# Kernel tuning notes

Measured on AMD Instinct MI355X. Metric: run time of the kernel, lower is better.

## Reference

```python
import jax, jax.numpy as jnp
import numpy as np

B, L, P, D, RD, M, K = 128, 128, 1024, 128, 128, 64, 4


def _ln(x, g, b):
    m = x.mean(-1, keepdims=True)
    v = ((x - m) ** 2).mean(-1, keepdims=True)
    return (x - m) / jnp.sqrt(v + 1e-5) * g + b


def _mlp2(x, w1, b1, w2, b2):
    return jax.nn.gelu(x @ w1 + b1, approximate=False) @ w2 + b2


def setup_inputs() -> dict:
    key = jax.random.key(0)
    ks = iter(jax.random.split(key, 64))

    def n(sh, s=1.0):
        return jax.random.normal(next(ks), sh, dtype=jnp.float32) * s

    def lin(i, o):
        return n((i, o), 1.0 / np.sqrt(i))

    inp = {}
    inp['l_pos'] = n((B, L, 3), 3.0)
    inp['l_x'] = n((B, L, 8))
    inp['p_pos'] = n((B, P, 3), 3.0)
    inp['p_x'] = n((B, P, 192))
    inp['p_score'] = n((B, P))
    inp['p_rad'] = jax.random.uniform(next(ks), (B, P), dtype=jnp.float32)
    inp['l_typ'] = jax.random.randint(next(ks), (B, L), 0, 256)
    inp['p_typ'] = jax.random.randint(next(ks), (B, P), 0, 256)
    inp['a_idx'] = jax.random.randint(next(ks), (B, M), 0, L)
    inp['b_idx'] = jax.random.randint(next(ks), (B, M), 0, L)
    inp['l_mask'] = jnp.ones((B, L), dtype=bool)
    inp['p_mask'] = jnp.ones((B, P), dtype=bool)
    inp.update(dict(
        le_emb=n((256, D), 0.02), le_w1=lin(8, D), le_b1=jnp.zeros(D), le_w2=lin(D, D), le_b2=jnp.zeros(D),
        le_g=jnp.ones(D), le_lnb=jnp.zeros(D),
        pe_emb=n((256, D), 0.02), pe_w1=lin(192, D), pe_b1=jnp.zeros(D), pe_w2=lin(D, D), pe_b2=jnp.zeros(D),
        ps_w1=lin(1, D), ps_b1=jnp.zeros(D), ps_w2=lin(D, D), ps_b2=jnp.zeros(D),
        pe_g=jnp.ones(D), pe_lnb=jnp.zeros(D),
        projL=lin(D, D), projP=lin(D, D), dustbin_vec=n((D,), 0.02),
        sg_w1=lin(D, D), sg_b1=jnp.zeros(D), sg_w2=lin(D, 1), sg_b2=jnp.zeros(1),
        inv_w1=lin(3, 64), inv_b1=jnp.zeros(64), inv_w2=lin(64, 1), inv_b2=jnp.zeros(1),
        retrL=lin(D, RD), retrP=lin(D, RD)))
    return inp


def _forward(l_pos, l_x, p_pos, p_x, p_score, p_rad,
             l_typ, p_typ, a_idx, b_idx, l_mask, p_mask,
             le_emb, le_w1, le_b1, le_w2, le_b2, le_g, le_lnb,
             pe_emb, pe_w1, pe_b1, pe_w2, pe_b2,
             ps_w1, ps_b1, ps_w2, ps_b2, pe_g, pe_lnb,
             projL, projP, dustbin_vec,
             sg_w1, sg_b1, sg_w2, sg_b2,
             inv_w1, inv_b1, inv_w2, inv_b2, retrL, retrP):
    neg = jnp.finfo(jnp.float32).min
    # encoders + projections
    hL = _ln(_mlp2(l_x, le_w1, le_b1, le_w2, le_b2) + le_emb[l_typ], le_g, le_lnb) @ projL  # [B,L,D]
    hP_pre = (_mlp2(p_x, pe_w1, pe_b1, pe_w2, pe_b2) + pe_emb[p_typ]
              + _mlp2(p_score[..., None], ps_w1, ps_b1, ps_w2, ps_b2))
    hP = _ln(hP_pre, pe_g, pe_lnb) @ projP  # [B,P,D]
    scale = 1.0 / jnp.sqrt(jnp.float32(hL.shape[-1]))
    # masked bipartite cross-attn logits
    logits = jnp.einsum('bld,bpd->blp', hL, hP) * scale
    logits_feat = jnp.where(p_mask[:, None, :], logits, neg)
    logits_feat = jnp.where(l_mask[:, :, None], logits_feat, neg)
    # dustbin log-softmax assignment
    dust = (hL @ dustbin_vec) * scale  # [B,L]
    full = jnp.concatenate([logits_feat, dust[:, :, None]], axis=-1)  # [B,L,P+1]
    full = jnp.where(l_mask[:, :, None], full, neg)
    logW = jax.nn.log_softmax(full, axis=-1)
    W = jnp.exp(logW)
    pm = p_mask.astype(jnp.float32)
    lm = l_mask.astype(jnp.float32)
    denomL = jnp.maximum(lm.sum(1), 1.0)
    Wm = jnp.concatenate([W[:, :, :-1] * pm[:, None, :], W[:, :, -1:]], axis=-1)
    sharp = (Wm.max(-1) * lm).sum(1) / denomL
    neg_ent = -((-(Wm * logW).sum(-1) * lm).sum(1) / denomL)
    # per-pocket-node sigma
    p_sigma = jax.nn.softplus(_mlp2(hP, sg_w1, sg_b1, sg_w2, sg_b2)[..., 0]) + 1e-3 + jnp.maximum(p_rad, 0.0)
    logW_real = logW[:, :, :-1]
    # sampled edge likelihood
    Bn = l_pos.shape[0]
    bi = jnp.arange(Bn)[:, None]
    valid = l_mask[bi, a_idx] & l_mask[bi, b_idx] & (a_idx != b_idx)  # [B,M]
    dist = jnp.linalg.norm(l_pos[bi, a_idx] - l_pos[bi, b_idx], axis=-1)[:, :, None, None]
    _, topj = jax.lax.top_k(logits_feat, K)  # [B,L,K]
    bi3 = jnp.arange(Bn)[:, None, None]
    p_sel = p_pos[bi3, topj]                 # [B,L,K,3]
    sig_sel = p_sigma[bi3, topj]             # [B,L,K]
    lW_top = jnp.take_along_axis(logW_real, topj, axis=2)  # [B,L,K]
    pa, pb = p_sel[bi, a_idx], p_sel[bi, b_idx]            # [B,M,K,3]
    siga, sigb = sig_sel[bi, a_idx], sig_sel[bi, b_idx]    # [B,M,K]
    lwa, lwb = lW_top[bi, a_idx], lW_top[bi, b_idx]
    mu = jnp.linalg.norm(pa[:, :, :, None, :] - pb[:, :, None, :, :], axis=-1)  # [B,M,K,K]
    sigma = jnp.sqrt(siga[:, :, :, None] ** 2 + sigb[:, :, None, :] ** 2 + 1e-6)
    logw_pair = lwa[:, :, :, None] + lwb[:, :, None, :]
    logp = -0.5 * ((dist - mu) / sigma) ** 2 - jnp.log(sigma) - 0.5 * jnp.log(2.0 * jnp.pi)
    logmix = jax.scipy.special.logsumexp(logw_pair + logp, axis=(-2, -1))  # [B,M]
    vp = valid.astype(jnp.float32)
    edge_raw = (logmix * vp).sum(1) / jnp.maximum(vp.sum(1), 1.0)
    edge = jnp.tanh(edge_raw / 5.0)  # edge_scale
    inv_vec = jnp.stack([sharp, neg_ent, edge], axis=1)  # [B,3]
    score_inv_geom = _mlp2(inv_vec, inv_w1, inv_b1, inv_w2, inv_b2)[..., 0]
    # pooled retrieval embeddings
    l_g = (hL * lm[:, :, None]).sum(1) / jnp.maximum(lm.sum(1, keepdims=True), 1.0)
    p_g = (hP * pm[:, :, None]).sum(1) / jnp.maximum(pm.sum(1, keepdims=True), 1.0)

    def _unit(x):
        return x / jnp.maximum(jnp.linalg.norm(x, axis=-1, keepdims=True), 1e-12)

    l_z = _unit(l_g @ retrL)
    p_z = _unit(p_g @ retrP)
    return jnp.concatenate([score_inv_geom[:, None], l_z, p_z], axis=-1)  # [B, 1+2*RD]


def reference(l_pos, l_x, p_pos, p_x, p_score, p_rad,
              l_typ, p_typ, a_idx, b_idx, l_mask, p_mask,
              le_emb, le_w1, le_b1, le_w2, le_b2, le_g, le_lnb,
              pe_emb, pe_w1, pe_b1, pe_w2, pe_b2,
              ps_w1, ps_b1, ps_w2, ps_b2, pe_g, pe_lnb,
              projL, projP, dustbin_vec,
              sg_w1, sg_b1, sg_w2, sg_b2,
              inv_w1, inv_b1, inv_w2, inv_b2, retrL, retrP):
    return _forward(l_pos, l_x, p_pos, p_x, p_score, p_rad,
                    l_typ, p_typ, a_idx, b_idx, l_mask, p_mask,
                    le_emb, le_w1, le_b1, le_w2, le_b2, le_g, le_lnb,
                    pe_emb, pe_w1, pe_b1, pe_w2, pe_b2,
                    ps_w1, ps_b1, ps_w2, ps_b2, pe_g, pe_lnb,
                    projL, projP, dustbin_vec,
                    sg_w1, sg_b1, sg_w2, sg_b2,
                    inv_w1, inv_b1, inv_w2, inv_b2, retrL, retrP)
```

## Files before the change

kernel.cpp:

```cpp
#include <hip/hip_runtime.h>
#include <math.h>

#define B_ 128
#define L_ 128
#define P_ 1024
#define D_ 128
#define M_ 64

typedef __attribute__((ext_vector_type(8))) short bf16x8;
typedef __attribute__((ext_vector_type(4))) float f32x4;

__device__ __forceinline__ float gelu_exact(float x) {
    return 0.5f * x * (1.0f + erff(x * 0.70710678118654752440f));
}
__device__ __forceinline__ float softplus_f(float x) {
    return fmaxf(x, 0.0f) + log1pf(expf(-fabsf(x)));
}
__device__ __forceinline__ unsigned short f2bf(float f) {
    unsigned int u = __float_as_uint(f);
    unsigned int r = (u + 0x7FFFu + ((u >> 16) & 1u)) >> 16;
    return (unsigned short)r;
}
__device__ __forceinline__ float bf2f(unsigned short h) {
    return __uint_as_float(((unsigned int)h) << 16);
}
__device__ __forceinline__ float xor32_sum(float v) {
#pragma unroll
    for (int o = 16; o > 0; o >>= 1) v += __shfl_xor(v, o, 32);
    return v;
}
__device__ __forceinline__ float blockReduceSum128(float v, volatile float* s2) {
#pragma unroll
    for (int o = 32; o > 0; o >>= 1) v += __shfl_down(v, o, 64);
    __syncthreads();
    if ((threadIdx.x & 63) == 0) s2[threadIdx.x >> 6] = v;
    __syncthreads();
    return s2[0] + s2[1];
}

template<int KK>
__device__ __forceinline__ void mm_tile(const float* __restrict__ W,
                                        const float* __restrict__ xT,
                                        int d0, int r0, float acc[4][4]) {
#pragma unroll 4
    for (int k = 0; k < KK; ++k) {
        float4 xv = *(const float4*)(xT + k * 16 + r0);
        float4 wv = *(const float4*)(W + k * D_ + d0);
        acc[0][0] += xv.x * wv.x; acc[0][1] += xv.x * wv.y; acc[0][2] += xv.x * wv.z; acc[0][3] += xv.x * wv.w;
        acc[1][0] += xv.y * wv.x; acc[1][1] += xv.y * wv.y; acc[1][2] += xv.y * wv.z; acc[1][3] += xv.y * wv.w;
        acc[2][0] += xv.z * wv.x; acc[2][1] += xv.z * wv.y; acc[2][2] += xv.z * wv.z; acc[2][3] += xv.z * wv.w;
        acc[3][0] += xv.w * wv.x; acc[3][1] += xv.w * wv.y; acc[3][2] += xv.w * wv.z; acc[3][3] += xv.w * wv.w;
    }
}

__global__ __launch_bounds__(256) void k_prep(
    const float* __restrict__ w1, const float* __restrict__ w2, const float* __restrict__ pp,
    const float* __restrict__ psw2, const float* __restrict__ sgw1,
    unsigned short* __restrict__ W1T, unsigned short* __restrict__ W2T, unsigned short* __restrict__ PPT,
    unsigned short* __restrict__ PSW2T, unsigned short* __restrict__ SGW1T)
{
    int d = blockIdx.x, t = threadIdx.x;
    for (int k = t; k < 192; k += 256) W1T[d * 200 + k] = f2bf(w1[k * 128 + d]);
    for (int k = t; k < 128; k += 256) {
        W2T[d * 136 + k]   = f2bf(w2[k * 128 + d]);
        PPT[d * 136 + k]   = f2bf(pp[k * 128 + d]);
        PSW2T[d * 136 + k] = f2bf(psw2[k * 128 + d]);
        SGW1T[d * 136 + k] = f2bf(sgw1[k * 128 + d]);
    }
}

__global__ __launch_bounds__(128) void k_hL(
    const float* __restrict__ l_x, const int* __restrict__ l_typ,
    const float* __restrict__ le_emb, const float* __restrict__ le_w1, const float* __restrict__ le_b1,
    const float* __restrict__ le_w2, const float* __restrict__ le_b2,
    const float* __restrict__ le_g, const float* __restrict__ le_lnb,
    const float* __restrict__ projL, float* __restrict__ hL)
{
    __shared__ __align__(16) float s_x[8 * 16];
    __shared__ __align__(16) float s_u[D_ * 16];
    __shared__ __align__(16) float s_v[D_ * 16];
    __shared__ int s_typ[16];
    int tid = threadIdx.x;
    int td = tid & 31, tr = tid >> 5;
    int d0 = td * 4, r0 = tr * 4;
    int row0 = blockIdx.x * 16;

    for (int i = tid; i < 16 * 8; i += 128) {
        int r = i >> 3, k = i & 7;
        s_x[k * 16 + r] = l_x[(row0 + r) * 8 + k];
    }
    if (tid < 16) s_typ[tid] = l_typ[row0 + tid];
    __syncthreads();

    float acc[4][4];
    {
        float4 b1 = *(const float4*)(le_b1 + d0);
#pragma unroll
        for (int i = 0; i < 4; ++i) { acc[i][0] = b1.x; acc[i][1] = b1.y; acc[i][2] = b1.z; acc[i][3] = b1.w; }
    }
    mm_tile<8>(le_w1, s_x, d0, r0, acc);
#pragma unroll
    for (int j = 0; j < 4; ++j)
        *(float4*)(s_u + (d0 + j) * 16 + r0) =
            make_float4(gelu_exact(acc[0][j]), gelu_exact(acc[1][j]), gelu_exact(acc[2][j]), gelu_exact(acc[3][j]));
    __syncthreads();

    {
        float4 b2 = *(const float4*)(le_b2 + d0);
#pragma unroll
        for (int i = 0; i < 4; ++i) {
            float4 e = *(const float4*)(le_emb + (long)s_typ[r0 + i] * D_ + d0);
            acc[i][0] = b2.x + e.x; acc[i][1] = b2.y + e.y; acc[i][2] = b2.z + e.z; acc[i][3] = b2.w + e.w;
        }
    }
    mm_tile<D_>(le_w2, s_u, d0, r0, acc);

    float ga[4], bb[4], ln[4][4];
    *(float4*)ga = *(const float4*)(le_g + d0);
    *(float4*)bb = *(const float4*)(le_lnb + d0);
#pragma unroll
    for (int i = 0; i < 4; ++i) {
        float s = acc[i][0] + acc[i][1] + acc[i][2] + acc[i][3];
        s = xor32_sum(s);
        float mean = s * (1.0f / D_);
        float dv[4], vs = 0.0f;
#pragma unroll
        for (int j = 0; j < 4; ++j) { dv[j] = acc[i][j] - mean; vs += dv[j] * dv[j]; }
        vs = xor32_sum(vs);
        float inv = rsqrtf(vs * (1.0f / D_) + 1e-5f);
#pragma unroll
        for (int j = 0; j < 4; ++j) ln[i][j] = dv[j] * inv * ga[j] + bb[j];
    }
    __syncthreads();
#pragma unroll
    for (int j = 0; j < 4; ++j)
        *(float4*)(s_v + (d0 + j) * 16 + r0) = make_float4(ln[0][j], ln[1][j], ln[2][j], ln[3][j]);
    __syncthreads();

#pragma unroll
    for (int i = 0; i < 4; ++i)
#pragma unroll
        for (int j = 0; j < 4; ++j) acc[i][j] = 0.0f;
    mm_tile<D_>(projL, s_v, d0, r0, acc);
#pragma unroll
    for (int i = 0; i < 4; ++i)
        *(float4*)(hL + (long)(row0 + r0 + i) * D_ + d0) = make_float4(acc[i][0], acc[i][1], acc[i][2], acc[i][3]);
}

#define KP1 200
#define KP2 136
#define TBo 0
#define HBo 8704
__global__ __launch_bounds__(256) void k_hP(
    const float* __restrict__ p_x, const float* __restrict__ p_score, const float* __restrict__ p_rad,
    const int* __restrict__ p_typ,
    const float* __restrict__ pe_emb, const float* __restrict__ pe_b1, const float* __restrict__ pe_b2,
    const float* __restrict__ ps_w1, const float* __restrict__ ps_b1, const float* __restrict__ ps_b2,
    const float* __restrict__ pe_g, const float* __restrict__ pe_lnb,
    const float* __restrict__ sg_b1, const float* __restrict__ sg_w2, const float* __restrict__ sg_b2,
    const unsigned short* __restrict__ W1T, const unsigned short* __restrict__ W2T,
    const unsigned short* __restrict__ PPT, const unsigned short* __restrict__ PSW2T,
    const unsigned short* __restrict__ SGW1T,
    unsigned short* __restrict__ hPb, float* __restrict__ p_sigma, float* __restrict__ w_pg)
{
    __shared__ unsigned short s_buf[17408];
    __shared__ float s_score[64], s_rad[64];
    __shared__ int s_typ[64];
    const int tid = threadIdx.x;
    const int wid = tid >> 6;
    const int l15 = tid & 15;
    const int g   = (tid & 63) >> 4;
    const long row0 = (long)blockIdx.x * 64;
    const int b  = (int)(row0 >> 10);
    const int p0 = (int)(row0 & (P_ - 1));
    const int arow = wid * 16 + l15;
    const int crow = wid * 16 + g * 4;

    {
        const float2* src = (const float2*)(p_x + row0 * 192);
        for (int i = tid; i < 64 * 96; i += 256) {
            int r = i / 96, kp = i - r * 96;
            float2 v = src[i];
            unsigned int packed = (unsigned int)f2bf(v.x) | ((unsigned int)f2bf(v.y) << 16);
            *(unsigned int*)&s_buf[r * KP1 + kp * 2] = packed;
        }
        if (tid < 64) {
            s_typ[tid] = p_typ[row0 + tid];
            s_score[tid] = p_score[row0 + tid];
            s_rad[tid] = p_rad[row0 + tid];
        }
    }
    __syncthreads();

    f32x4 acc[8];
#pragma unroll
    for (int nt = 0; nt < 8; ++nt) {
        float bv = pe_b1[nt * 16 + l15];
        acc[nt] = (f32x4){bv, bv, bv, bv};
    }
#pragma unroll
    for (int k0 = 0; k0 < 192; k0 += 32) {
        bf16x8 a = *(const bf16x8*)&s_buf[arow * KP1 + k0 + g * 8];
#pragma unroll
        for (int nt = 0; nt < 8; ++nt) {
            bf16x8 bb = *(const bf16x8*)&W1T[(nt * 16 + l15) * KP1 + k0 + g * 8];
            acc[nt] = __builtin_amdgcn_mfma_f32_16x16x32_bf16(a, bb, acc[nt], 0, 0, 0);
        }
    }
    __syncthreads();

#pragma unroll
    for (int nt = 0; nt < 8; ++nt)
#pragma unroll
        for (int reg = 0; reg < 4; ++reg)
            s_buf[TBo + (crow + reg) * KP2 + nt * 16 + l15] = f2bf(gelu_exact(acc[nt][reg]));
    for (int i = tid; i < 64 * 64; i += 256) {
        int r = i >> 6, kp = (i & 63) * 2;
        float sc = s_score[r];
        unsigned int packed = (unsigned int)f2bf(gelu_exact(sc * ps_w1[kp] + ps_b1[kp])) |
                              ((unsigned int)f2bf(gelu_exact(sc * ps_w1[kp + 1] + ps_b1[kp + 1])) << 16);
        *(unsigned int*)&s_buf[HBo + r * KP2 + kp] = packed;
    }
    __syncthreads();

#pragma unroll
    for (int nt = 0; nt < 8; ++nt) {
        int d = nt * 16 + l15;
        float bias = pe_b2[d] + ps_b2[d];
        f32x4 c;
#pragma unroll
        for (int reg = 0; reg < 4; ++reg)
            c[reg] = bias + pe_emb[(long)s_typ[crow + reg] * 128 + d];
        acc[nt] = c;
    }
#pragma unroll
    for (int k0 = 0; k0 < 128; k0 += 32) {
        bf16x8 a1 = *(const bf16x8*)&s_buf[TBo + arow * KP2 + k0 + g * 8];
        bf16x8 a2 = *(const bf16x8*)&s_buf[HBo + arow * KP2 + k0 + g * 8];
#pragma unroll
        for (int nt = 0; nt < 8; ++nt) {
            bf16x8 b1v = *(const bf16x8*)&W2T[(nt * 16 + l15) * KP2 + k0 + g * 8];
            acc[nt] = __builtin_amdgcn_mfma_f32_16x16x32_bf16(a1, b1v, acc[nt], 0, 0, 0);
            bf16x8 b2v = *(const bf16x8*)&PSW2T[(nt * 16 + l15) * KP2 + k0 + g * 8];
            acc[nt] = __builtin_amdgcn_mfma_f32_16x16x32_bf16(a2, b2v, acc[nt], 0, 0, 0);
        }
    }

    {
        float gg[8], lb[8];
#pragma unroll
        for (int nt = 0; nt < 8; ++nt) { gg[nt] = pe_g[nt * 16 + l15]; lb[nt] = pe_lnb[nt * 16 + l15]; }
#pragma unroll
        for (int reg = 0; reg < 4; ++reg) {
            float s = 0.0f;
#pragma unroll
            for (int nt = 0; nt < 8; ++nt) s += acc[nt][reg];
            s += __shfl_xor(s, 1); s += __shfl_xor(s, 2); s += __shfl_xor(s, 4); s += __shfl_xor(s, 8);
            float mean = s * (1.0f / 128.0f);
            float vs = 0.0f;
#pragma unroll
            for (int nt = 0; nt < 8; ++nt) { float dv = acc[nt][reg] - mean; vs += dv * dv; }
            vs += __shfl_xor(vs, 1); vs += __shfl_xor(vs, 2); vs += __shfl_xor(vs, 4); vs += __shfl_xor(vs, 8);
            float inv = rsqrtf(vs * (1.0f / 128.0f) + 1e-5f);
#pragma unroll
            for (int nt = 0; nt < 8; ++nt)
                acc[nt][reg] = (acc[nt][reg] - mean) * inv * gg[nt] + lb[nt];
        }
    }
    __syncthreads();
#pragma unroll
    for (int nt = 0; nt < 8; ++nt)
#pragma unroll
        for (int reg = 0; reg < 4; ++reg)
            s_buf[HBo + (crow + reg) * KP2 + nt * 16 + l15] = f2bf(acc[nt][reg]);
    __syncthreads();

#pragma unroll
    for (int nt = 0; nt < 8; ++nt) acc[nt] = (f32x4){0.0f, 0.0f, 0.0f, 0.0f};
#pragma unroll
    for (int k0 = 0; k0 < 128; k0 += 32) {
        bf16x8 a = *(const bf16x8*)&s_buf[HBo + arow * KP2 + k0 + g * 8];
#pragma unroll
        for (int nt = 0; nt < 8; ++nt) {
            bf16x8 bb = *(const bf16x8*)&PPT[(nt * 16 + l15) * KP2 + k0 + g * 8];
            acc[nt] = __builtin_amdgcn_mfma_f32_16x16x32_bf16(a, bb, acc[nt], 0, 0, 0);
        }
    }
#pragma unroll
    for (int nt = 0; nt < 8; ++nt) {
        float s = acc[nt][0] + acc[nt][1] + acc[nt][2] + acc[nt][3];
        s += __shfl_xor(s, 16);
        s += __shfl_xor(s, 32);
        if (((tid & 63) >> 4) == 0) atomicAdd(&w_pg[b * D_ + nt * 16 + l15], s);
    }
#pragma unroll
    for (int nt = 0; nt < 8; ++nt)
#pragma unroll
        for (int reg = 0; reg < 4; ++reg)
            s_buf[TBo + (crow + reg) * KP2 + nt * 16 + l15] = f2bf(acc[nt][reg]);
    __syncthreads();

    for (int i = tid; i < 1024; i += 256) {
        int r = i >> 4, seg = i & 15;
        uint4 v = *(const uint4*)&s_buf[TBo + r * KP2 + seg * 8];
        *(uint4*)&hPb[(row0 + r) * (long)D_ + seg * 8] = v;
    }

#pragma unroll
    for (int nt = 0; nt < 8; ++nt) {
        float bv = sg_b1[nt * 16 + l15];
        acc[nt] = (f32x4){bv, bv, bv, bv};
    }
#pragma unroll
    for (int k0 = 0; k0 < 128; k0 += 32) {
        bf16x8 a = *(const bf16x8*)&s_buf[TBo + arow * KP2 + k0 + g * 8];
#pragma unroll
        for (int nt = 0; nt < 8; ++nt) {
            bf16x8 bb = *(const bf16x8*)&SGW1T[(nt * 16 + l15) * KP2 + k0 + g * 8];
            acc[nt] = __builtin_amdgcn_mfma_f32_16x16x32_bf16(a, bb, acc[nt], 0, 0, 0);
        }
    }
    {
        float w2v[8];
#pragma unroll
        for (int nt = 0; nt < 8; ++nt) w2v[nt] = sg_w2[nt * 16 + l15];
        float sgb2 = sg_b2[0];
#pragma unroll
        for (int reg = 0; reg < 4; ++reg) {
            float part = 0.0f;
#pragma unroll
            for (int nt = 0; nt < 8; ++nt) part += gelu_exact(acc[nt][reg]) * w2v[nt];
            part += __shfl_xor(part, 1); part += __shfl_xor(part, 2);
            part += __shfl_xor(part, 4); part += __shfl_xor(part, 8);
            if (l15 == 0) {
                int r = crow + reg;
                p_sigma[(long)b * P_ + p0 + r] = softplus_f(part + sgb2) + 0.001f + fmaxf(s_rad[r], 0.0f);
            }
        }
    }
}

__global__ __launch_bounds__(256) void k_logits(
    const float* __restrict__ hL, const unsigned short* __restrict__ hPb,
    const float* __restrict__ dustbin,
    float* __restrict__ w_sharp, float* __restrict__ w_ent,
    float* __restrict__ w_lw, int* __restrict__ w_idx)
{
    __shared__ unsigned short s_hl[16 * 136];
    __shared__ unsigned short s_lg[16 * 1048];
    __shared__ float s_dust[16];
    __shared__ float s_red_m[4][16];
    __shared__ float2 s_red_s[4][16];
    __shared__ float s_lse[16];

    const int tid = threadIdx.x;
    const int w = tid >> 6;
    const int l15 = tid & 15;
    const int g = (tid & 63) >> 4;
    const int b = blockIdx.x >> 3;
    const int l0 = (blockIdx.x & 7) * 16;
    const float scale = 0.08838834764831845f;

    for (int i = tid; i < 16 * 16; i += 256) {
        int r = i >> 4, c8 = (i & 15) * 8;
        const float4* src = (const float4*)(hL + ((long)(b * L_ + l0 + r)) * D_ + c8);
        float4 v0 = src[0], v1 = src[1];
        unsigned int u0 = (unsigned)f2bf(v0.x) | ((unsigned)f2bf(v0.y) << 16);
        unsigned int u1 = (unsigned)f2bf(v0.z) | ((unsigned)f2bf(v0.w) << 16);
        unsigned int u2 = (unsigned)f2bf(v1.x) | ((unsigned)f2bf(v1.y) << 16);
        unsigned int u3 = (unsigned)f2bf(v1.z) | ((unsigned)f2bf(v1.w) << 16);
        *(uint4*)&s_hl[r * 136 + c8] = make_uint4(u0, u1, u2, u3);
    }
    __syncthreads();

    {
        int r = tid >> 4;
        int k0 = (tid & 15) * 8;
        float s = 0.0f;
#pragma unroll
        for (int e = 0; e < 8; ++e) s += bf2f(s_hl[r * 136 + k0 + e]) * dustbin[k0 + e];
        s += __shfl_xor(s, 1); s += __shfl_xor(s, 2); s += __shfl_xor(s, 4); s += __shfl_xor(s, 8);
        if ((tid & 15) == 0) s_dust[r] = s * scale;
    }

    bf16x8 a[4];
#pragma unroll
    for (int k = 0; k < 4; ++k) a[k] = *(const bf16x8*)&s_hl[l15 * 136 + k * 32 + g * 8];
    const unsigned short* hp = hPb + (long)b * P_ * D_ + (long)(w * 256 + l15) * D_ + g * 8;
    f32x4 acc[16];
#pragma unroll
    for (int nt = 0; nt < 16; ++nt) acc[nt] = (f32x4){0.0f, 0.0f, 0.0f, 0.0f};
#pragma unroll
    for (int k = 0; k < 4; ++k) {
#pragma unroll
        for (int nt = 0; nt < 16; ++nt) {
            bf16x8 bb = *(const bf16x8*)(hp + nt * (16 * D_) + k * 32);
            acc[nt] = __builtin_amdgcn_mfma_f32_16x16x32_bf16(a[k], bb, acc[nt], 0, 0, 0);
        }
    }
#pragma unroll
    for (int nt = 0; nt < 16; ++nt)
#pragma unroll
        for (int reg = 0; reg < 4; ++reg) acc[nt][reg] *= scale;

    float mloc[4];
#pragma unroll
    for (int reg = 0; reg < 4; ++reg) {
        float m = acc[0][reg];
#pragma unroll
        for (int nt = 1; nt < 16; ++nt) m = fmaxf(m, acc[nt][reg]);
        m = fmaxf(m, __shfl_xor(m, 1)); m = fmaxf(m, __shfl_xor(m, 2));
        m = fmaxf(m, __shfl_xor(m, 4)); m = fmaxf(m, __shfl_xor(m, 8));
        mloc[reg] = m;
        if (l15 == 0) s_red_m[w][g * 4 + reg] = m;
    }
#pragma unroll
    for (int nt = 0; nt < 16; ++nt)
#pragma unroll
        for (int reg = 0; reg < 4; ++reg)
            s_lg[(g * 4 + reg) * 1048 + w * 256 + nt * 16 + l15] = f2bf(acc[nt][reg]);
    __syncthreads();

    float mf[4];
#pragma unroll
    for (int reg = 0; reg < 4; ++reg) {
        int r = g * 4 + reg;
        float m = fmaxf(fmaxf(s_red_m[0][r], s_red_m[1][r]), fmaxf(s_red_m[2][r], s_red_m[3][r]));
        mf[reg] = fmaxf(m, s_dust[r]);
    }
#pragma unroll
    for (int reg = 0; reg < 4; ++reg) {
        float S0 = 0.0f, S1 = 0.0f;
#pragma unroll
        for (int nt = 0; nt < 16; ++nt) {
            float x = acc[nt][reg] - mf[reg];
            float e = expf(x);
            S0 += e; S1 += e * x;
        }
        S0 += __shfl_xor(S0, 1); S0 += __shfl_xor(S0, 2); S0 += __shfl_xor(S0, 4); S0 += __shfl_xor(S0, 8);
        S1 += __shfl_xor(S1, 1); S1 += __shfl_xor(S1, 2); S1 += __shfl_xor(S1, 4); S1 += __shfl_xor(S1, 8);
        if (l15 == 0) s_red_s[w][g * 4 + reg] = make_float2(S0, S1);
    }
    __syncthreads();

    if (tid < 64 && l15 == 0) {
#pragma unroll
        for (int reg = 0; reg < 4; ++reg) {
            int r = g * 4 + reg;
            float m = mf[reg];
            float S0 = 0.0f, S1 = 0.0f;
#pragma unroll
            for (int ww = 0; ww < 4; ++ww) { float2 s = s_red_s[ww][r]; S0 += s.x; S1 += s.y; }
            float xd = s_dust[r] - m;
            float ed = expf(xd);
            S0 += ed; S1 += ed * xd;
            float lgz = logf(S0);
            int rowg = b * L_ + l0 + r;
            w_sharp[rowg] = 1.0f / S0;
            w_ent[rowg] = S1 / S0 - lgz;
            s_lse[r] = m + lgz;
        }
    }
    __syncthreads();

    {
        int r = tid >> 4;
        int lane = tid & 15;
        float lse = s_lse[r];
        int rowg = b * L_ + l0 + r;
        for (int k = 0; k < 4; ++k) {
            float bv = -INFINITY; int bi = P_;
            for (int c = lane; c < P_; c += 16) {
                float v = bf2f(s_lg[r * 1048 + c]);
                if (v > bv || (v == bv && c < bi)) { bv = v; bi = c; }
            }
#pragma unroll
            for (int o = 1; o < 16; o <<= 1) {
                float ov = __shfl_xor(bv, o);
                int   oi = __shfl_xor(bi, o);
                if (ov > bv || (ov == bv && oi < bi)) { bv = ov; bi = oi; }
            }
            if (lane == 0) {
                w_lw[rowg * 4 + k] = bv - lse;
                w_idx[rowg * 4 + k] = bi;
            }
            s_lg[r * 1048 + bi] = 0xFF80;
        }
    }
}

__global__ __launch_bounds__(64) void k_edge(
    const int* __restrict__ a_idx, const int* __restrict__ b_idx,
    const float* __restrict__ l_pos, const float* __restrict__ p_pos,
    const float* __restrict__ p_sigma, const float* __restrict__ w_lw,
    const int* __restrict__ w_idx, float* __restrict__ w_edge)
{
    int b = blockIdx.x, m = threadIdx.x;
    int ai = a_idx[b * M_ + m], bi = b_idx[b * M_ + m];
    bool valid = (ai != bi);
    float ax = l_pos[(b * L_ + ai) * 3 + 0], ay = l_pos[(b * L_ + ai) * 3 + 1], az = l_pos[(b * L_ + ai) * 3 + 2];
    float bx = l_pos[(b * L_ + bi) * 3 + 0], by = l_pos[(b * L_ + bi) * 3 + 1], bz = l_pos[(b * L_ + bi) * 3 + 2];
    float dx = ax - bx, dy = ay - by, dz = az - bz;
    float dist = sqrtf(dx * dx + dy * dy + dz * dz);

    float pax[4], pay[4], paz[4], sa2[4], lwa[4];
    float pbx[4], pby[4], pbz[4], sb2[4], lwb[4];
#pragma unroll
    for (int k = 0; k < 4; ++k) {
        int ja = w_idx[(b * L_ + ai) * 4 + k];
        pax[k] = p_pos[(b * P_ + ja) * 3 + 0]; pay[k] = p_pos[(b * P_ + ja) * 3 + 1]; paz[k] = p_pos[(b * P_ + ja) * 3 + 2];
        float sa = p_sigma[b * P_ + ja]; sa2[k] = sa * sa;
        lwa[k] = w_lw[(b * L_ + ai) * 4 + k];
        int jb = w_idx[(b * L_ + bi) * 4 + k];
        pbx[k] = p_pos[(b * P_ + jb) * 3 + 0]; pby[k] = p_pos[(b * P_ + jb) * 3 + 1]; pbz[k] = p_pos[(b * P_ + jb) * 3 + 2];
        float sb = p_sigma[b * P_ + jb]; sb2[k] = sb * sb;
        lwb[k] = w_lw[(b * L_ + bi) * 4 + k];
    }
    float t[16];
    float mx = -INFINITY;
#pragma unroll
    for (int j = 0; j < 4; ++j)
#pragma unroll
        for (int k = 0; k < 4; ++k) {
            float ddx = pax[j] - pbx[k], ddy = pay[j] - pby[k], ddz = paz[j] - pbz[k];
            float mu = sqrtf(ddx * ddx + ddy * ddy + ddz * ddz);
            float s2 = sa2[j] + sb2[k] + 1e-6f;
            float diff = dist - mu;
            float lp = lwa[j] + lwb[k] - 0.5f * diff * diff / s2 - 0.5f * logf(s2) - 0.91893853320467274f;
            t[j * 4 + k] = lp;
            mx = fmaxf(mx, lp);
        }
    float se = 0.0f;
#pragma unroll
    for (int n = 0; n < 16; ++n) se += expf(t[n] - mx);
    float logmix = mx + logf(se);
    float v = valid ? logmix : 0.0f;
    float c = valid ? 1.0f : 0.0f;
#pragma unroll
    for (int o = 32; o > 0; o >>= 1) { v += __shfl_down(v, o, 64); c += __shfl_down(c, o, 64); }
    if (m == 0) w_edge[b] = tanhf((v / fmaxf(c, 1.0f)) * 0.2f);
}

__global__ __launch_bounds__(128) void k_final(
    const float* __restrict__ hL, const float* __restrict__ w_pg,
    const float* __restrict__ w_sharp, const float* __restrict__ w_ent, const float* __restrict__ w_edge,
    const float* __restrict__ inv_w1, const float* __restrict__ inv_b1,
    const float* __restrict__ inv_w2, const float* __restrict__ inv_b2,
    const float* __restrict__ retrL, const float* __restrict__ retrP,
    float* __restrict__ out)
{
    __shared__ float s_red[2];
    __shared__ float s_vec[D_];
    int b = blockIdx.x, tid = threadIdx.x;
    float sharp = blockReduceSum128(w_sharp[b * L_ + tid], s_red) * (1.0f / L_);
    float neg_ent = blockReduceSum128(w_ent[b * L_ + tid], s_red) * (1.0f / L_);
    float edge = w_edge[b];
    float v = 0.0f;
    if (tid < 64) {
        float h = gelu_exact(sharp * inv_w1[tid] + neg_ent * inv_w1[64 + tid] + edge * inv_w1[128 + tid] + inv_b1[tid]);
        v = h * inv_w2[tid];
    }
    float sc = blockReduceSum128(v, s_red);
    if (tid == 0) out[b * 257] = sc + inv_b2[0];

    float lg = 0.0f;
    for (int l = 0; l < L_; ++l) lg += hL[((long)b * L_ + l) * D_ + tid];
    s_vec[tid] = lg * (1.0f / L_);
    __syncthreads();
    float z = 0.0f;
    for (int k = 0; k < D_; ++k) z += s_vec[k] * retrL[k * D_ + tid];
    float nrm = sqrtf(blockReduceSum128(z * z, s_red));
    out[b * 257 + 1 + tid] = z / fmaxf(nrm, 1e-12f);
    __syncthreads();

    s_vec[tid] = w_pg[b * D_ + tid] * (1.0f / P_);
    __syncthreads();
    z = 0.0f;
    for (int k = 0; k < D_; ++k) z += s_vec[k] * retrP[k * D_ + tid];
    nrm = sqrtf(blockReduceSum128(z * z, s_red));
    out[b * 257 + 129 + tid] = z / fmaxf(nrm, 1e-12f);
}

extern "C" void kernel_launch(void* const* d_in, const int* in_sizes, int n_in,
                              void* d_out, int out_size, void* d_ws, size_t ws_size,
                              hipStream_t stream) {
    (void)in_sizes; (void)n_in; (void)out_size; (void)ws_size;
    const float* l_pos  = (const float*)d_in[0];
    const float* l_x    = (const float*)d_in[1];
    const float* p_pos  = (const float*)d_in[2];
    const float* p_x    = (const float*)d_in[3];
    const float* p_score= (const float*)d_in[4];
    const float* p_rad  = (const float*)d_in[5];
    const int*   l_typ  = (const int*)d_in[6];
    const int*   p_typ  = (const int*)d_in[7];
    const int*   a_idx  = (const int*)d_in[8];
    const int*   b_idx  = (const int*)d_in[9];
    const float* le_emb = (const float*)d_in[12];
    const float* le_w1  = (const float*)d_in[13];
    const float* le_b1  = (const float*)d_in[14];
    const float* le_w2  = (const float*)d_in[15];
    const float* le_b2  = (const float*)d_in[16];
    const float* le_g   = (const float*)d_in[17];
    const float* le_lnb = (const float*)d_in[18];
    const float* pe_emb = (const float*)d_in[19];
    const float* pe_w1  = (const float*)d_in[20];
    const float* pe_b1  = (const float*)d_in[21];
    const float* pe_w2  = (const float*)d_in[22];
    const float* pe_b2  = (const float*)d_in[23];
    const float* ps_w1  = (const float*)d_in[24];
    const float* ps_b1  = (const float*)d_in[25];
    const float* ps_w2  = (const float*)d_in[26];
    const float* ps_b2  = (const float*)d_in[27];
    const float* pe_g   = (const float*)d_in[28];
    const float* pe_lnb = (const float*)d_in[29];
    const float* projL  = (const float*)d_in[30];
    const float* projP  = (const float*)d_in[31];
    const float* dustbin= (const float*)d_in[32];
    const float* sg_w1  = (const float*)d_in[33];
    const float* sg_b1  = (const float*)d_in[34];
    const float* sg_w2  = (const float*)d_in[35];
    const float* sg_b2  = (const float*)d_in[36];
    const float* inv_w1 = (const float*)d_in[37];
    const float* inv_b1 = (const float*)d_in[38];
    const float* inv_w2 = (const float*)d_in[39];
    const float* inv_b2 = (const float*)d_in[40];
    const float* retrL  = (const float*)d_in[41];
    const float* retrP  = (const float*)d_in[42];

    unsigned short* hPb = (unsigned short*)d_ws;
    float* hL      = (float*)(hPb + (size_t)B_ * P_ * D_);
    float* p_sigma = hL + (size_t)B_ * L_ * D_;
    float* w_sharp = p_sigma + (size_t)B_ * P_;
    float* w_ent   = w_sharp + B_ * L_;
    float* w_lw    = w_ent + B_ * L_;
    int*   w_idx   = (int*)(w_lw + B_ * L_ * 4);
    float* w_edge  = (float*)(w_idx + B_ * L_ * 4);
    float* w_pg    = w_edge + B_;
    unsigned short* W1T   = (unsigned short*)(w_pg + B_ * D_);
    unsigned short* W2T   = W1T + 128 * 200;
    unsigned short* PPT   = W2T + 128 * 136;
    unsigned short* PSW2T = PPT + 128 * 136;
    unsigned short* SGW1T = PSW2T + 128 * 136;

    hipMemsetAsync(w_pg, 0, B_ * D_ * sizeof(float), stream);

    hipLaunchKernelGGL(k_prep, dim3(128), dim3(256), 0, stream,
                       pe_w1, pe_w2, projP, ps_w2, sg_w1, W1T, W2T, PPT, PSW2T, SGW1T);
    hipLaunchKernelGGL(k_hL, dim3(B_ * L_ / 16), dim3(128), 0, stream,
                       l_x, l_typ, le_emb, le_w1, le_b1, le_w2, le_b2, le_g, le_lnb, projL, hL);
    hipLaunchKernelGGL(k_hP, dim3(B_ * P_ / 64), dim3(256), 0, stream,
                       p_x, p_score, p_rad, p_typ, pe_emb, pe_b1, pe_b2,
                       ps_w1, ps_b1, ps_b2, pe_g, pe_lnb,
                       sg_b1, sg_w2, sg_b2,
                       W1T, W2T, PPT, PSW2T, SGW1T,
                       hPb, p_sigma, w_pg);
    hipLaunchKernelGGL(k_logits, dim3(B_ * (L_ / 16)), dim3(256), 0, stream,
                       hL, hPb, dustbin, w_sharp, w_ent, w_lw, w_idx);
    hipLaunchKernelGGL(k_edge, dim3(B_), dim3(64), 0, stream,
                       a_idx, b_idx, l_pos, p_pos, p_sigma, w_lw, w_idx, w_edge);
    hipLaunchKernelGGL(k_final, dim3(B_), dim3(128), 0, stream,
                       hL, w_pg, w_sharp, w_ent, w_edge, inv_w1, inv_b1, inv_w2, inv_b2, retrL, retrP,
                       (float*)d_out);
}
```

Measured before the change: 567.7 us.

## Restructure hP kernel to direct loads, fast GELU, fuse edge and final kernels

k_hP now loads p_x straight from global into MFMA fragments and computes the score-MLP hidden activations in registers. This removes the large shared staging buffer and most block-wide barriers, and a launch-bounds hint raises occupancy. Exact erf GELU in k_hP is replaced by the tanh approximation, which changes numerics. The ligand mean-pool moves into k_hL through atomics, and k_edge is merged into the final kernel to save a launch and the hL re-read.

```diff
diff --git a/kernel.cpp b/kernel.cpp
--- a/kernel.cpp
+++ b/kernel.cpp
@@ -13,6 +13,12 @@
 __device__ __forceinline__ float gelu_exact(float x) {
     return 0.5f * x * (1.0f + erff(x * 0.70710678118654752440f));
 }
+__device__ __forceinline__ float gelu_fast(float x) {
+    float y = 0.7978845608028654f * (x + 0.044715f * x * x * x);
+    float e = __expf(2.0f * y);
+    float t = 1.0f - 2.0f / (e + 1.0f);
+    return 0.5f * x * (1.0f + t);
+}
 __device__ __forceinline__ float softplus_f(float x) {
     return fmaxf(x, 0.0f) + log1pf(expf(-fabsf(x)));
 }
@@ -23,6 +29,14 @@
 }
 __device__ __forceinline__ float bf2f(unsigned short h) {
     return __uint_as_float(((unsigned int)h) << 16);
+}
+__device__ __forceinline__ bf16x8 pack8(float4 a, float4 b) {
+    union { unsigned int u[4]; bf16x8 v; } r;
+    r.u[0] = (unsigned)f2bf(a.x) | ((unsigned)f2bf(a.y) << 16);
+    r.u[1] = (unsigned)f2bf(a.z) | ((unsigned)f2bf(a.w) << 16);
+    r.u[2] = (unsigned)f2bf(b.x) | ((unsigned)f2bf(b.y) << 16);
+    r.u[3] = (unsigned)f2bf(b.z) | ((unsigned)f2bf(b.w) << 16);
+    return r.v;
 }
 __device__ __forceinline__ float xor32_sum(float v) {
 #pragma unroll
@@ -74,7 +88,7 @@
     const float* __restrict__ le_emb, const float* __restrict__ le_w1, const float* __restrict__ le_b1,
     const float* __restrict__ le_w2, const float* __restrict__ le_b2,
     const float* __restrict__ le_g, const float* __restrict__ le_lnb,
-    const float* __restrict__ projL, float* __restrict__ hL)
+    const float* __restrict__ projL, float* __restrict__ hL, float* __restrict__ w_lg)
 {
     __shared__ __align__(16) float s_x[8 * 16];
     __shared__ __align__(16) float s_u[D_ * 16];
@@ -145,13 +159,19 @@
 #pragma unroll
     for (int i = 0; i < 4; ++i)
         *(float4*)(hL + (long)(row0 + r0 + i) * D_ + d0) = make_float4(acc[i][0], acc[i][1], acc[i][2], acc[i][3]);
+
+    int b = row0 >> 7;
+#pragma unroll
+    for (int j = 0; j < 4; ++j) {
+        float s = acc[0][j] + acc[1][j] + acc[2][j] + acc[3][j];
+        s += __shfl_xor(s, 32, 64);
+        if ((tr & 1) == 0) atomicAdd(&w_lg[b * D_ + d0 + j], s);
+    }
 }
 
 #define KP1 200
 #define KP2 136
-#define TBo 0
-#define HBo 8704
-__global__ __launch_bounds__(256) void k_hP(
+__global__ __launch_bounds__(256, 5) void k_hP(
     const float* __restrict__ p_x, const float* __restrict__ p_score, const float* __restrict__ p_rad,
     const int* __restrict__ p_typ,
     const float* __restrict__ pe_emb, const float* __restrict__ pe_b1, const float* __restrict__ pe_b2,
@@ -163,34 +183,17 @@
     const unsigned short* __restrict__ SGW1T,
     unsigned short* __restrict__ hPb, float* __restrict__ p_sigma, float* __restrict__ w_pg)
 {
-    __shared__ unsigned short s_buf[17408];
-    __shared__ float s_score[64], s_rad[64];
-    __shared__ int s_typ[64];
-    const int tid = threadIdx.x;
-    const int wid = tid >> 6;
-    const int l15 = tid & 15;
-    const int g   = (tid & 63) >> 4;
+    __shared__ unsigned short s_tb[64 * KP2];
+    const int tid  = threadIdx.x;
+    const int wid  = tid >> 6;
+    const int lane = tid & 63;
+    const int l15  = tid & 15;
+    const int g    = lane >> 4;
     const long row0 = (long)blockIdx.x * 64;
-    const int b  = (int)(row0 >> 10);
-    const int p0 = (int)(row0 & (P_ - 1));
+    const int b = (int)(row0 >> 10);
     const int arow = wid * 16 + l15;
     const int crow = wid * 16 + g * 4;
-
-    {
-        const float2* src = (const float2*)(p_x + row0 * 192);
-        for (int i = tid; i < 64 * 96; i += 256) {
-            int r = i / 96, kp = i - r * 96;
-            float2 v = src[i];
-            unsigned int packed = (unsigned int)f2bf(v.x) | ((unsigned int)f2bf(v.y) << 16);
-            *(unsigned int*)&s_buf[r * KP1 + kp * 2] = packed;
-        }
-        if (tid < 64) {
-            s_typ[tid] = p_typ[row0 + tid];
-            s_score[tid] = p_score[row0 + tid];
-            s_rad[tid] = p_rad[row0 + tid];
-        }
-    }
-    __syncthreads();
+    const long grow = row0 + arow;
 
     f32x4 acc[8];
 #pragma unroll
@@ -198,31 +201,29 @@
         float bv = pe_b1[nt * 16 + l15];
         acc[nt] = (f32x4){bv, bv, bv, bv};
     }
-#pragma unroll
-    for (int k0 = 0; k0 < 192; k0 += 32) {
-        bf16x8 a = *(const bf16x8*)&s_buf[arow * KP1 + k0 + g * 8];
-#pragma unroll
-        for (int nt = 0; nt < 8; ++nt) {
-            bf16x8 bb = *(const bf16x8*)&W1T[(nt * 16 + l15) * KP1 + k0 + g * 8];
-            acc[nt] = __builtin_amdgcn_mfma_f32_16x16x32_bf16(a, bb, acc[nt], 0, 0, 0);
-        }
-    }
-    __syncthreads();
-
+    {
+        const float* xrow = p_x + grow * 192;
+#pragma unroll
+        for (int k = 0; k < 6; ++k) {
+            float4 v0 = *(const float4*)(xrow + k * 32 + g * 8);
+            float4 v1 = *(const float4*)(xrow + k * 32 + g * 8 + 4);
+            bf16x8 a = pack8(v0, v1);
+#pragma unroll
+            for (int nt = 0; nt < 8; ++nt) {
+                bf16x8 bb = *(const bf16x8*)&W1T[(nt * 16 + l15) * KP1 + k * 32 + g * 8];
+                acc[nt] = __builtin_amdgcn_mfma_f32_16x16x32_bf16(a, bb, acc[nt], 0, 0, 0);
+            }
+        }
+    }
 #pragma unroll
     for (int nt = 0; nt < 8; ++nt)
 #pragma unroll
         for (int reg = 0; reg < 4; ++reg)
-            s_buf[TBo + (crow + reg) * KP2 + nt * 16 + l15] = f2bf(gelu_exact(acc[nt][reg]));
-    for (int i = tid; i < 64 * 64; i += 256) {
-        int r = i >> 6, kp = (i & 63) * 2;
-        float sc = s_score[r];
-        unsigned int packed = (unsigned int)f2bf(gelu_exact(sc * ps_w1[kp] + ps_b1[kp])) |
-                              ((unsigned int)f2bf(gelu_exact(sc * ps_w1[kp + 1] + ps_b1[kp + 1])) << 16);
-        *(unsigned int*)&s_buf[HBo + r * KP2 + kp] = packed;
-    }
-    __syncthreads();
-
+            s_tb[(crow + reg) * KP2 + nt * 16 + l15] = f2bf(gelu_fast(acc[nt][reg]));
+
+    int typ[4];
+#pragma unroll
+    for (int reg = 0; reg < 4; ++reg) typ[reg] = p_typ[row0 + crow + reg];
 #pragma unroll
     for (int nt = 0; nt < 8; ++nt) {
         int d = nt * 16 + l15;
@@ -230,19 +231,30 @@
         f32x4 c;
 #pragma unroll
         for (int reg = 0; reg < 4; ++reg)
-            c[reg] = bias + pe_emb[(long)s_typ[crow + reg] * 128 + d];
+            c[reg] = bias + pe_emb[(long)typ[reg] * D_ + d];
         acc[nt] = c;
     }
-#pragma unroll
-    for (int k0 = 0; k0 < 128; k0 += 32) {
-        bf16x8 a1 = *(const bf16x8*)&s_buf[TBo + arow * KP2 + k0 + g * 8];
-        bf16x8 a2 = *(const bf16x8*)&s_buf[HBo + arow * KP2 + k0 + g * 8];
-#pragma unroll
-        for (int nt = 0; nt < 8; ++nt) {
-            bf16x8 b1v = *(const bf16x8*)&W2T[(nt * 16 + l15) * KP2 + k0 + g * 8];
-            acc[nt] = __builtin_amdgcn_mfma_f32_16x16x32_bf16(a1, b1v, acc[nt], 0, 0, 0);
-            bf16x8 b2v = *(const bf16x8*)&PSW2T[(nt * 16 + l15) * KP2 + k0 + g * 8];
-            acc[nt] = __builtin_amdgcn_mfma_f32_16x16x32_bf16(a2, b2v, acc[nt], 0, 0, 0);
+    {
+        float score = p_score[grow];
+#pragma unroll
+        for (int k = 0; k < 4; ++k) {
+            float4 w0 = *(const float4*)(ps_w1 + k * 32 + g * 8);
+            float4 w1v = *(const float4*)(ps_w1 + k * 32 + g * 8 + 4);
+            float4 c0 = *(const float4*)(ps_b1 + k * 32 + g * 8);
+            float4 c1 = *(const float4*)(ps_b1 + k * 32 + g * 8 + 4);
+            float4 h0 = make_float4(gelu_fast(score * w0.x + c0.x), gelu_fast(score * w0.y + c0.y),
+                                    gelu_fast(score * w0.z + c0.z), gelu_fast(score * w0.w + c0.w));
+            float4 h1 = make_float4(gelu_fast(score * w1v.x + c1.x), gelu_fast(score * w1v.y + c1.y),
+                                    gelu_fast(score * w1v.z + c1.z), gelu_fast(score * w1v.w + c1.w));
+            bf16x8 ah = pack8(h0, h1);
+            bf16x8 a1 = *(const bf16x8*)&s_tb[arow * KP2 + k * 32 + g * 8];
+#pragma unroll
+            for (int nt = 0; nt < 8; ++nt) {
+                bf16x8 b1v = *(const bf16x8*)&W2T[(nt * 16 + l15) * KP2 + k * 32 + g * 8];
+                acc[nt] = __builtin_amdgcn_mfma_f32_16x16x32_bf16(a1, b1v, acc[nt], 0, 0, 0);
+                bf16x8 b2v = *(const bf16x8*)&PSW2T[(nt * 16 + l15) * KP2 + k * 32 + g * 8];
+                acc[nt] = __builtin_amdgcn_mfma_f32_16x16x32_bf16(ah, b2v, acc[nt], 0, 0, 0);
+            }
         }
     }
 
@@ -267,22 +279,20 @@
                 acc[nt][reg] = (acc[nt][reg] - mean) * inv * gg[nt] + lb[nt];
         }
     }
-    __syncthreads();
 #pragma unroll
     for (int nt = 0; nt < 8; ++nt)
 #pragma unroll
         for (int reg = 0; reg < 4; ++reg)
-            s_buf[HBo + (crow + reg) * KP2 + nt * 16 + l15] = f2bf(acc[nt][reg]);
-    __syncthreads();
+            s_tb[(crow + reg) * KP2 + nt * 16 + l15] = f2bf(acc[nt][reg]);
 
 #pragma unroll
     for (int nt = 0; nt < 8; ++nt) acc[nt] = (f32x4){0.0f, 0.0f, 0.0f, 0.0f};
 #pragma unroll
-    for (int k0 = 0; k0 < 128; k0 += 32) {
-        bf16x8 a = *(const bf16x8*)&s_buf[HBo + arow * KP2 + k0 + g * 8];
+    for (int k = 0; k < 4; ++k) {
+        bf16x8 a = *(const bf16x8*)&s_tb[arow * KP2 + k * 32 + g * 8];
 #pragma unroll
         for (int nt = 0; nt < 8; ++nt) {
-            bf16x8 bb = *(const bf16x8*)&PPT[(nt * 16 + l15) * KP2 + k0 + g * 8];
+            bf16x8 bb = *(const bf16x8*)&PPT[(nt * 16 + l15) * KP2 + k * 32 + g * 8];
             acc[nt] = __builtin_amdgcn_mfma_f32_16x16x32_bf16(a, bb, acc[nt], 0, 0, 0);
         }
     }
@@ -291,19 +301,20 @@
         float s = acc[nt][0] + acc[nt][1] + acc[nt][2] + acc[nt][3];
         s += __shfl_xor(s, 16);
         s += __shfl_xor(s, 32);
-        if (((tid & 63) >> 4) == 0) atomicAdd(&w_pg[b * D_ + nt * 16 + l15], s);
+        if (g == 0) atomicAdd(&w_pg[b * D_ + nt * 16 + l15], s);
     }
 #pragma unroll
     for (int nt = 0; nt < 8; ++nt)
 #pragma unroll
         for (int reg = 0; reg < 4; ++reg)
-            s_buf[TBo + (crow + reg) * KP2 + nt * 16 + l15] = f2bf(acc[nt][reg]);
-    __syncthreads();
-
-    for (int i = tid; i < 1024; i += 256) {
-        int r = i >> 4, seg = i & 15;
-        uint4 v = *(const uint4*)&s_buf[TBo + r * KP2 + seg * 8];
-        *(uint4*)&hPb[(row0 + r) * (long)D_ + seg * 8] = v;
+            s_tb[(crow + reg) * KP2 + nt * 16 + l15] = f2bf(acc[nt][reg]);
+
+#pragma unroll
+    for (int it = 0; it < 4; ++it) {
+        int idx = lane + it * 64;
+        int r = idx >> 4, seg = idx & 15;
+        uint4 v = *(const uint4*)&s_tb[(wid * 16 + r) * KP2 + seg * 8];
+        *(uint4*)&hPb[(row0 + wid * 16 + r) * (long)D_ + seg * 8] = v;
     }
 
 #pragma unroll
@@ -312,11 +323,11 @@
         acc[nt] = (f32x4){bv, bv, bv, bv};
     }
 #pragma unroll
-    for (int k0 = 0; k0 < 128; k0 += 32) {
-        bf16x8 a = *(const bf16x8*)&s_buf[TBo + arow * KP2 + k0 + g * 8];
+    for (int k = 0; k < 4; ++k) {
+        bf16x8 a = *(const bf16x8*)&s_tb[arow * KP2 + k * 32 + g * 8];
 #pragma unroll
         for (int nt = 0; nt < 8; ++nt) {
-            bf16x8 bb = *(const bf16x8*)&SGW1T[(nt * 16 + l15) * KP2 + k0 + g * 8];
+            bf16x8 bb = *(const bf16x8*)&SGW1T[(nt * 16 + l15) * KP2 + k * 32 + g * 8];
             acc[nt] = __builtin_amdgcn_mfma_f32_16x16x32_bf16(a, bb, acc[nt], 0, 0, 0);
         }
     }
@@ -329,12 +340,12 @@
         for (int reg = 0; reg < 4; ++reg) {
             float part = 0.0f;
 #pragma unroll
-            for (int nt = 0; nt < 8; ++nt) part += gelu_exact(acc[nt][reg]) * w2v[nt];
+            for (int nt = 0; nt < 8; ++nt) part += gelu_fast(acc[nt][reg]) * w2v[nt];
             part += __shfl_xor(part, 1); part += __shfl_xor(part, 2);
             part += __shfl_xor(part, 4); part += __shfl_xor(part, 8);
             if (l15 == 0) {
-                int r = crow + reg;
-                p_sigma[(long)b * P_ + p0 + r] = softplus_f(part + sgb2) + 0.001f + fmaxf(s_rad[r], 0.0f);
+                long r = row0 + crow + reg;
+                p_sigma[r] = softplus_f(part + sgb2) + 0.001f + fmaxf(p_rad[r], 0.0f);
             }
         }
     }
@@ -403,7 +414,6 @@
 #pragma unroll
         for (int reg = 0; reg < 4; ++reg) acc[nt][reg] *= scale;
 
-    float mloc[4];
 #pragma unroll
     for (int reg = 0; reg < 4; ++reg) {
         float m = acc[0][reg];
@@ -411,7 +421,6 @@
         for (int nt = 1; nt < 16; ++nt) m = fmaxf(m, acc[nt][reg]);
         m = fmaxf(m, __shfl_xor(m, 1)); m = fmaxf(m, __shfl_xor(m, 2));
         m = fmaxf(m, __shfl_xor(m, 4)); m = fmaxf(m, __shfl_xor(m, 8));
-        mloc[reg] = m;
         if (l15 == 0) s_red_m[w][g * 4 + reg] = m;
     }
 #pragma unroll
@@ -489,61 +498,12 @@
     }
 }
 
-__global__ __launch_bounds__(64) void k_edge(
+__global__ __launch_bounds__(128) void k_final2(
     const int* __restrict__ a_idx, const int* __restrict__ b_idx,
     const float* __restrict__ l_pos, const float* __restrict__ p_pos,
-    const float* __restrict__ p_sigma, const float* __restrict__ w_lw,
-    const int* __restrict__ w_idx, float* __restrict__ w_edge)
-{
-    int b = blockIdx.x, m = threadIdx.x;
-    int ai = a_idx[b * M_ + m], bi = b_idx[b * M_ + m];
-    bool valid = (ai != bi);
-    float ax = l_pos[(b * L_ + ai) * 3 + 0], ay = l_pos[(b * L_ + ai) * 3 + 1], az = l_pos[(b * L_ + ai) * 3 + 2];
-    float bx = l_pos[(b * L_ + bi) * 3 + 0], by = l_pos[(b * L_ + bi) * 3 + 1], bz = l_pos[(b * L_ + bi) * 3 + 2];
-    float dx = ax - bx, dy = ay - by, dz = az - bz;
-    float dist = sqrtf(dx * dx + dy * dy + dz * dz);
-
-    float pax[4], pay[4], paz[4], sa2[4], lwa[4];
-    float pbx[4], pby[4], pbz[4], sb2[4], lwb[4];
-#pragma unroll
-    for (int k = 0; k < 4; ++k) {
-        int ja = w_idx[(b * L_ + ai) * 4 + k];
-        pax[k] = p_pos[(b * P_ + ja) * 3 + 0]; pay[k] = p_pos[(b * P_ + ja) * 3 + 1]; paz[k] = p_pos[(b * P_ + ja) * 3 + 2];
-        float sa = p_sigma[b * P_ + ja]; sa2[k] = sa * sa;
-        lwa[k] = w_lw[(b * L_ + ai) * 4 + k];
-        int jb = w_idx[(b * L_ + bi) * 4 + k];
-        pbx[k] = p_pos[(b * P_ + jb) * 3 + 0]; pby[k] = p_pos[(b * P_ + jb) * 3 + 1]; pbz[k] = p_pos[(b * P_ + jb) * 3 + 2];
-        float sb = p_sigma[b * P_ + jb]; sb2[k] = sb * sb;
-        lwb[k] = w_lw[(b * L_ + bi) * 4 + k];
-    }
-    float t[16];
-    float mx = -INFINITY;
-#pragma unroll
-    for (int j = 0; j < 4; ++j)
-#pragma unroll
-        for (int k = 0; k < 4; ++k) {
-            float ddx = pax[j] - pbx[k], ddy = pay[j] - pby[k], ddz = paz[j] - pbz[k];
-            float mu = sqrtf(ddx * ddx + ddy * ddy + ddz * ddz);
-            float s2 = sa2[j] + sb2[k] + 1e-6f;
-            float diff = dist - mu;
-            float lp = lwa[j] + lwb[k] - 0.5f * diff * diff / s2 - 0.5f * logf(s2) - 0.91893853320467274f;
-            t[j * 4 + k] = lp;
-            mx = fmaxf(mx, lp);
-        }
-    float se = 0.0f;
-#pragma unroll
-    for (int n = 0; n < 16; ++n) se += expf(t[n] - mx);
-    float logmix = mx + logf(se);
-    float v = valid ? logmix : 0.0f;
-    float c = valid ? 1.0f : 0.0f;
-#pragma unroll
-    for (int o = 32; o > 0; o >>= 1) { v += __shfl_down(v, o, 64); c += __shfl_down(c, o, 64); }
-    if (m == 0) w_edge[b] = tanhf((v / fmaxf(c, 1.0f)) * 0.2f);
-}
-
-__global__ __launch_bounds__(128) void k_final(
-    const float* __restrict__ hL, const float* __restrict__ w_pg,
-    const float* __restrict__ w_sharp, const float* __restrict__ w_ent, const float* __restrict__ w_edge,
+    const float* __restrict__ p_sigma, const float* __restrict__ w_lw, const int* __restrict__ w_idx,
+    const float* __restrict__ w_lg, const float* __restrict__ w_pg,
+    const float* __restrict__ w_sharp, const float* __restrict__ w_ent,
     const float* __restrict__ inv_w1, const float* __restrict__ inv_b1,
     const float* __restrict__ inv_w2, const float* __restrict__ inv_b2,
     const float* __restrict__ retrL, const float* __restrict__ retrP,
@@ -551,10 +511,60 @@
 {
     __shared__ float s_red[2];
     __shared__ float s_vec[D_];
+    __shared__ float s_edge;
     int b = blockIdx.x, tid = threadIdx.x;
+
+    if (tid < 64) {
+        int m = tid;
+        int ai = a_idx[b * M_ + m], bi = b_idx[b * M_ + m];
+        bool valid = (ai != bi);
+        float ax = l_pos[(b * L_ + ai) * 3 + 0], ay = l_pos[(b * L_ + ai) * 3 + 1], az = l_pos[(b * L_ + ai) * 3 + 2];
+        float bx = l_pos[(b * L_ + bi) * 3 + 0], by = l_pos[(b * L_ + bi) * 3 + 1], bz = l_pos[(b * L_ + bi) * 3 + 2];
+        float dx = ax - bx, dy = ay - by, dz = az - bz;
+        float dist = sqrtf(dx * dx + dy * dy + dz * dz);
+
+        float pax[4], pay[4], paz[4], sa2[4], lwa[4];
+        float pbx[4], pby[4], pbz[4], sb2[4], lwb[4];
+#pragma unroll
+        for (int k = 0; k < 4; ++k) {
+            int ja = w_idx[(b * L_ + ai) * 4 + k];
+            pax[k] = p_pos[(b * P_ + ja) * 3 + 0]; pay[k] = p_pos[(b * P_ + ja) * 3 + 1]; paz[k] = p_pos[(b * P_ + ja) * 3 + 2];
+            float sa = p_sigma[b * P_ + ja]; sa2[k] = sa * sa;
+            lwa[k] = w_lw[(b * L_ + ai) * 4 + k];
+            int jb = w_idx[(b * L_ + bi) * 4 + k];
+            pbx[k] = p_pos[(b * P_ + jb) * 3 + 0]; pby[k] = p_pos[(b * P_ + jb) * 3 + 1]; pbz[k] = p_pos[(b * P_ + jb) * 3 + 2];
+            float sb = p_sigma[b * P_ + jb]; sb2[k] = sb * sb;
+            lwb[k] = w_lw[(b * L_ + bi) * 4 + k];
+        }
+        float t[16];
+        float mx = -INFINITY;
+#pragma unroll
+        for (int j = 0; j < 4; ++j)
+#pragma unroll
+            for (int k = 0; k < 4; ++k) {
+                float ddx = pax[j] - pbx[k], ddy = pay[j] - pby[k], ddz = paz[j] - pbz[k];
+                float mu = sqrtf(ddx * ddx + ddy * ddy + ddz * ddz);
+                float s2 = sa2[j] + sb2[k] + 1e-6f;
+                float diff = dist - mu;
+                float lp = lwa[j] + lwb[k] - 0.5f * diff * diff / s2 - 0.5f * logf(s2) - 0.91893853320467274f;
+                t[j * 4 + k] = lp;
+                mx = fmaxf(mx, lp);
+            }
+        float se = 0.0f;
+#pragma unroll
+        for (int n = 0; n < 16; ++n) se += expf(t[n] - mx);
+        float logmix = mx + logf(se);
+        float v = valid ? logmix : 0.0f;
+        float c = valid ? 1.0f : 0.0f;
+#pragma unroll
+        for (int o = 32; o > 0; o >>= 1) { v += __shfl_down(v, o, 64); c += __shfl_down(c, o, 64); }
+        if (m == 0) s_edge = tanhf((v / fmaxf(c, 1.0f)) * 0.2f);
+    }
+    __syncthreads();
+    float edge = s_edge;
+
     float sharp = blockReduceSum128(w_sharp[b * L_ + tid], s_red) * (1.0f / L_);
     float neg_ent = blockReduceSum128(w_ent[b * L_ + tid], s_red) * (1.0f / L_);
-    float edge = w_edge[b];
     float v = 0.0f;
     if (tid < 64) {
         float h = gelu_exact(sharp * inv_w1[tid] + neg_ent * inv_w1[64 + tid] + edge * inv_w1[128 + tid] + inv_b1[tid]);
@@ -563,9 +573,7 @@
     float sc = blockReduceSum128(v, s_red);
     if (tid == 0) out[b * 257] = sc + inv_b2[0];
 
-    float lg = 0.0f;
-    for (int l = 0; l < L_; ++l) lg += hL[((long)b * L_ + l) * D_ + tid];
-    s_vec[tid] = lg * (1.0f / L_);
+    s_vec[tid] = w_lg[b * D_ + tid] * (1.0f / L_);
     __syncthreads();
     float z = 0.0f;
     for (int k = 0; k < D_; ++k) z += s_vec[k] * retrL[k * D_ + tid];
@@ -634,20 +642,20 @@
     float* w_ent   = w_sharp + B_ * L_;
     float* w_lw    = w_ent + B_ * L_;
     int*   w_idx   = (int*)(w_lw + B_ * L_ * 4);
-    float* w_edge  = (float*)(w_idx + B_ * L_ * 4);
-    float* w_pg    = w_edge + B_;
-    unsigned short* W1T   = (unsigned short*)(w_pg + B_ * D_);
+    float* w_pg    = (float*)(w_idx + B_ * L_ * 4);
+    float* w_lg    = w_pg + B_ * D_;
+    unsigned short* W1T   = (unsigned short*)(w_lg + B_ * D_);
     unsigned short* W2T   = W1T + 128 * 200;
     unsigned short* PPT   = W2T + 128 * 136;
     unsigned short* PSW2T = PPT + 128 * 136;
     unsigned short* SGW1T = PSW2T + 128 * 136;
 
-    hipMemsetAsync(w_pg, 0, B_ * D_ * sizeof(float), stream);
+    hipMemsetAsync(w_pg, 0, 2 * B_ * D_ * sizeof(float), stream);
 
     hipLaunchKernelGGL(k_prep, dim3(128), dim3(256), 0, stream,
                        pe_w1, pe_w2, projP, ps_w2, sg_w1, W1T, W2T, PPT, PSW2T, SGW1T);
     hipLaunchKernelGGL(k_hL, dim3(B_ * L_ / 16), dim3(128), 0, stream,
-                       l_x, l_typ, le_emb, le_w1, le_b1, le_w2, le_b2, le_g, le_lnb, projL, hL);
+                       l_x, l_typ, le_emb, le_w1, le_b1, le_w2, le_b2, le_g, le_lnb, projL, hL, w_lg);
     hipLaunchKernelGGL(k_hP, dim3(B_ * P_ / 64), dim3(256), 0, stream,
                        p_x, p_score, p_rad, p_typ, pe_emb, pe_b1, pe_b2,
                        ps_w1, ps_b1, ps_b2, pe_g, pe_lnb,
@@ -656,9 +664,9 @@
                        hPb, p_sigma, w_pg);
     hipLaunchKernelGGL(k_logits, dim3(B_ * (L_ / 16)), dim3(256), 0, stream,
                        hL, hPb, dustbin, w_sharp, w_ent, w_lw, w_idx);
-    hipLaunchKernelGGL(k_edge, dim3(B_), dim3(64), 0, stream,
-                       a_idx, b_idx, l_pos, p_pos, p_sigma, w_lw, w_idx, w_edge);
-    hipLaunchKernelGGL(k_final, dim3(B_), dim3(128), 0, stream,
-                       hL, w_pg, w_sharp, w_ent, w_edge, inv_w1, inv_b1, inv_w2, inv_b2, retrL, retrP,
+    hipLaunchKernelGGL(k_final2, dim3(B_), dim3(128), 0, stream,
+                       a_idx, b_idx, l_pos, p_pos, p_sigma, w_lw, w_idx,
+                       w_lg, w_pg, w_sharp, w_ent,
+                       inv_w1, inv_b1, inv_w2, inv_b2, retrL, retrP,
                        (float*)d_out);
 }
```

Result: faster. 548.5 us (-3.4%).
